# Kernel optimization log

Hardware: AMD Instinct MI355X
Metric: run time of the kernel (lower is better)

The kernel has to match this reference:

```python
import jax, jax.numpy as jnp
import numpy as np
from jax import lax

N_ANCHOR = 9
FEAT_STRIDE = 16
N_PRE_NMS = 2000
N_POST_NMS = 300
NMS_THRESH = 0.7
MIN_SIZE = 16.0
SCALE = 1.0


def generate_anchor(feat_stride, h, w):
    # base anchors: scales {8,16,32} x ratios {0.5,1,2}, (y1,x1,y2,x2)
    base = float(feat_stride)
    ratios = jnp.array([0.5, 1.0, 2.0], jnp.float32)
    scales = jnp.array([8.0, 16.0, 32.0], jnp.float32)
    py = px = base / 2.0
    hs = base * scales[None, :] * jnp.sqrt(ratios)[:, None]          # [3,3]
    ws = base * scales[None, :] * jnp.sqrt(1.0 / ratios)[:, None]    # [3,3]
    anchor_base = jnp.stack([py - hs / 2, px - ws / 2, py + hs / 2, px + ws / 2], axis=-1).reshape(9, 4)
    shift_y = jnp.arange(h, dtype=jnp.float32) * feat_stride
    shift_x = jnp.arange(w, dtype=jnp.float32) * feat_stride
    sy, sx = jnp.meshgrid(shift_y, shift_x, indexing='ij')
    shifts = jnp.stack([sy, sx, sy, sx], axis=-1).reshape(-1, 1, 4)  # [h*w,1,4]
    return (shifts + anchor_base[None]).reshape(-1, 4)               # [h*w*9,4]


def loc2bbox(anchor, loc):
    ah = anchor[:, 2] - anchor[:, 0]
    aw = anchor[:, 3] - anchor[:, 1]
    acy = anchor[:, 0] + 0.5 * ah
    acx = anchor[:, 1] + 0.5 * aw
    dy, dx, dh, dw = loc[:, 0], loc[:, 1], loc[:, 2], loc[:, 3]
    cy = dy * ah + acy
    cx = dx * aw + acx
    h = jnp.exp(dh) * ah
    w = jnp.exp(dw) * aw
    return jnp.stack([cy - 0.5 * h, cx - 0.5 * w, cy + 0.5 * h, cx + 0.5 * w], axis=1)


def nms_keep(boxes, thresh):
    # boxes sorted by descending score; returns keep mask
    y1, x1, y2, x2 = boxes[:, 0], boxes[:, 1], boxes[:, 2], boxes[:, 3]
    area = (y2 - y1) * (x2 - x1)
    yy1 = jnp.maximum(y1[:, None], y1[None, :])
    xx1 = jnp.maximum(x1[:, None], x1[None, :])
    yy2 = jnp.minimum(y2[:, None], y2[None, :])
    xx2 = jnp.minimum(x2[:, None], x2[None, :])
    inter = jnp.clip(yy2 - yy1, 0.0) * jnp.clip(xx2 - xx1, 0.0)
    iou = inter / (area[:, None] + area[None, :] - inter + 1e-9)
    n = boxes.shape[0]

    def step(supp, i):
        keep_i = jnp.logical_not(supp[i])
        supp = supp | (keep_i & (iou[i] > thresh))
        return supp, keep_i

    _, keep = lax.scan(step, jnp.zeros((n,), bool), jnp.arange(n))
    return keep


def proposal_single(loc, score, anchor, img_h, img_w):
    roi = loc2bbox(anchor, loc)
    roi = jnp.stack([
        jnp.clip(roi[:, 0], 0.0, img_h),
        jnp.clip(roi[:, 1], 0.0, img_w),
        jnp.clip(roi[:, 2], 0.0, img_h),
        jnp.clip(roi[:, 3], 0.0, img_w)], axis=1)
    hs = roi[:, 2] - roi[:, 0]
    ws = roi[:, 3] - roi[:, 1]
    ms = MIN_SIZE * SCALE
    score = jnp.where((hs >= ms) & (ws >= ms), score, -jnp.inf)
    top_s, idx = lax.top_k(score, N_PRE_NMS)
    boxes = roi[idx]
    keep = nms_keep(boxes, NMS_THRESH) & jnp.isfinite(top_s)
    order = jnp.argsort(jnp.logical_not(keep), stable=True)[:N_POST_NMS]
    out = boxes[order]
    kout = keep[order]
    return jnp.where(kout[:, None], out, 0.0), kout


def _conv(x, w, b, pad):
    y = lax.conv_general_dilated(x, w, (1, 1), pad, dimension_numbers=('NCHW', 'OIHW', 'NCHW'))
    return y + b[None, :, None, None]


def setup_inputs() -> dict:
    key = jax.random.key(0)
    ks = jax.random.split(key, 7)
    n, c, h, w = 8, 512, 64, 64
    x = jax.random.normal(ks[0], (n, c, h, w), jnp.float32)
    conv_w = 0.01 * jax.random.normal(ks[1], (512, c, 3, 3), jnp.float32)
    conv_b = 0.01 * jax.random.normal(ks[2], (512,), jnp.float32)
    score_w = 0.01 * jax.random.normal(ks[3], (2 * N_ANCHOR, 512, 1, 1), jnp.float32)
    score_b = 0.01 * jax.random.normal(ks[4], (2 * N_ANCHOR,), jnp.float32)
    params_w = 0.01 * jax.random.normal(ks[5], (4 * N_ANCHOR, 512, 1, 1), jnp.float32)
    params_b = 0.01 * jax.random.normal(ks[6], (4 * N_ANCHOR,), jnp.float32)
    return {"x": x, "conv_w": conv_w, "conv_b": conv_b, "score_w": score_w, "score_b": score_b,
            "params_w": params_w, "params_b": params_b, "img_h": 1024, "img_w": 1024}


def reference(x, conv_w, conv_b, score_w, score_b, params_w, params_b, img_h, img_w):
    n, _, h, w = x.shape
    anchor = generate_anchor(FEAT_STRIDE, h, w)                       # [h*w*9,4]
    mid = jax.nn.relu(_conv(x, conv_w, conv_b, 'SAME'))               # [n,512,h,w]
    rpn_params = _conv(mid, params_w, params_b, 'VALID')              # [n,36,h,w]
    rpn_params = rpn_params.transpose(0, 2, 3, 1).reshape(n, -1, 4)   # [n,h*w*9,4]
    rpn_score = _conv(mid, score_w, score_b, 'VALID')                 # [n,18,h,w]
    rpn_score = rpn_score.transpose(0, 2, 3, 1).reshape(n, -1, 2)     # [n,h*w*9,2]
    fg_score = jax.nn.softmax(rpn_score, axis=2)[:, :, 1]             # [n,h*w*9]
    rois, keep = jax.vmap(lambda l, s: proposal_single(l, s, anchor, float(img_h), float(img_w)))(rpn_params, fg_score)
    roi_index = jnp.repeat(jnp.arange(n, dtype=jnp.int32), N_POST_NMS)
    rois = rois.reshape(-1, 4)
    return rpn_params, rpn_score, rois, roi_index, anchor


if __name__ == '__main__':
    out = reference(**setup_inputs())
    print([o.shape for o in out])
```

## Files before the change

### kernel.cpp

```cpp
#include <hip/hip_runtime.h>
#include <math.h>

typedef _Float16 f16x8 __attribute__((ext_vector_type(8)));
typedef float f32x4 __attribute__((ext_vector_type(4)));
typedef unsigned long long u64;

#define OUT_PARAMS 0L
#define OUT_SCORE  1179648L
#define OUT_ROIS   1769472L
#define OUT_IDX    1779072L
#define OUT_ANCH   1781472L

#define WS_WT2   0L
#define WS_W2H   27648L
#define WS_W2L   1207296L
#define WS_XT    2386944L
#define WS_MID   19164160L
#define WS_FG    35941376L
#define WS_KEYS  36236288L
#define WS_BOX   36531200L
#define WS_SELK  37710848L
#define WS_SBOX  37727232L
#define WS_SUPP  37792768L

__global__ void k_transpose_w(const float* __restrict__ conv_w,
                              const float* __restrict__ score_w,
                              const float* __restrict__ params_w,
                              _Float16* __restrict__ W2h, _Float16* __restrict__ W2l,
                              float* __restrict__ wt2) {
  int e = blockIdx.x * 256 + threadIdx.x;
  if (e < 9 * 512 * 512) {
    int tap = e >> 18, rem = e & 262143;
    int oc = rem >> 9, c = rem & 511;
    float v = conv_w[(oc * 512 + c) * 9 + tap] * 1024.0f;
    _Float16 h = (_Float16)v;
    W2h[e] = h;
    W2l[e] = (_Float16)(v - (float)h);
  }
  if (e < 512 * 54) {
    int o = e % 54, c = e / 54;
    wt2[e] = (o < 18) ? score_w[o * 512 + c] : params_w[(o - 18) * 512 + c];
  }
}

__global__ __launch_bounds__(256) void k_split_x(const float* __restrict__ x,
                                                 float* __restrict__ Xt) {
  __shared__ float t[64][66];
  const int pxb = blockIdx.x;
  const int c0  = blockIdx.y * 64;
  const int n   = blockIdx.z;
  const int tid = threadIdx.x;
  const int a = tid >> 6, b = tid & 63;
#pragma unroll
  for (int i = 0; i < 16; ++i) {
    int c_l = i * 4 + a;
    t[c_l][b] = x[((size_t)(n * 512 + c0 + c_l) * 4096) + pxb * 64 + b];
  }
  __syncthreads();
#pragma unroll
  for (int i = 0; i < 16; ++i) {
    int px_l = i * 4 + a;
    Xt[((size_t)(n * 4096 + pxb * 64 + px_l) * 512) + c0 + b] = t[b][px_l];
  }
}

__global__ __launch_bounds__(256, 2) void k_conv_mfma(
    const float* __restrict__ Xt, const _Float16* __restrict__ W2h,
    const _Float16* __restrict__ W2l, const float* __restrict__ bias,
    float* __restrict__ mid) {
  __shared__ _Float16 XH[8448];
  __shared__ _Float16 XL[8448];

  const int n   = blockIdx.x >> 5;
  const int rp  = blockIdx.x & 31;
  const int oc0 = blockIdx.y * 128;
  const int tid = threadIdx.x;
  const int lane = tid & 63, wid = tid >> 6;
  const int wm = wid >> 1, wn = wid & 1;
  const int l15 = lane & 15, kg = lane >> 4;

  f32x4 acch[4][4], accl[4][4];
#pragma unroll
  for (int i = 0; i < 4; ++i)
#pragma unroll
    for (int j = 0; j < 4; ++j) {
      acch[i][j] = (f32x4){0.f, 0.f, 0.f, 0.f};
      accl[i][j] = (f32x4){0.f, 0.f, 0.f, 0.f};
    }

  for (int cb = 0; cb < 16; ++cb) {
    __syncthreads();
    for (int u = tid; u < 1056; u += 256) {
      const int px = u >> 2, sd = u & 3;
      const int cg = sd ^ ((px >> 1) & 3);
      const int hrow = px / 66, hcol = px - hrow * 66;
      const int y = rp * 2 - 1 + hrow, xx = hcol - 1;
      float4 v0 = {0.f, 0.f, 0.f, 0.f}, v1 = {0.f, 0.f, 0.f, 0.f};
      if ((unsigned)y < 64u && (unsigned)xx < 64u) {
        const float* s = Xt + (((size_t)(n * 64 + y) * 64 + xx) * 512 + cb * 32 + cg * 8);
        v0 = *(const float4*)s;
        v1 = *(const float4*)(s + 4);
      }
      f16x8 hv, lv;
      float f[8] = {v0.x, v0.y, v0.z, v0.w, v1.x, v1.y, v1.z, v1.w};
#pragma unroll
      for (int e = 0; e < 8; ++e) {
        const float fs = f[e] * 512.0f;
        _Float16 h = (_Float16)fs;
        hv[e] = h;
        lv[e] = (_Float16)(fs - (float)h);
      }
      *(f16x8*)(XH + u * 8) = hv;
      *(f16x8*)(XL + u * 8) = lv;
    }
    __syncthreads();

#pragma unroll
    for (int ky = 0; ky < 3; ++ky) {
#pragma unroll
      for (int kx = 0; kx < 3; ++kx) {
        const int tap = ky * 3 + kx;
        f16x8 ah[4], al[4], bh[4], bl[4];
#pragma unroll
        for (int mf = 0; mf < 4; ++mf) {
          const size_t aoff =
              ((size_t)(tap * 512 + oc0 + wm * 64 + mf * 16 + l15)) * 512 + cb * 32 + kg * 8;
          ah[mf] = *(const f16x8*)(W2h + aoff);
          al[mf] = *(const f16x8*)(W2l + aoff);
        }
#pragma unroll
        for (int nf = 0; nf < 4; ++nf) {
          const int lpx = (wn + ky) * 66 + nf * 16 + l15 + kx;
          const int off = lpx * 32 + ((kg ^ ((lpx >> 1) & 3)) * 8);
          bh[nf] = *(const f16x8*)(XH + off);
          bl[nf] = *(const f16x8*)(XL + off);
        }
#pragma unroll
        for (int mf = 0; mf < 4; ++mf)
#pragma unroll
          for (int nf = 0; nf < 4; ++nf) {
            acch[mf][nf] = __builtin_amdgcn_mfma_f32_16x16x32_f16(ah[mf], bh[nf], acch[mf][nf], 0, 0, 0);
            accl[mf][nf] = __builtin_amdgcn_mfma_f32_16x16x32_f16(ah[mf], bl[nf], accl[mf][nf], 0, 0, 0);
            accl[mf][nf] = __builtin_amdgcn_mfma_f32_16x16x32_f16(al[mf], bh[nf], accl[mf][nf], 0, 0, 0);
          }
      }
    }
  }

  const float inv = 1.0f / (1024.0f * 512.0f);
  const int y = rp * 2 + wn;
#pragma unroll
  for (int mf = 0; mf < 4; ++mf) {
#pragma unroll
    for (int r = 0; r < 4; ++r) {
      const int oc = oc0 + wm * 64 + mf * 16 + kg * 4 + r;
      const float bv = bias[oc];
      float* mp = mid + (((size_t)(n * 512 + oc) * 64 + y) * 64);
#pragma unroll
      for (int nf = 0; nf < 4; ++nf) {
        const int xcol = nf * 16 + l15;
        mp[xcol] = fmaxf((acch[mf][nf][r] + accl[mf][nf][r]) * inv + bv, 0.f);
      }
    }
  }
}

__global__ __launch_bounds__(256) void k_1x1(
    const float* __restrict__ mid, const float* __restrict__ wt2,
    const float* __restrict__ score_b, const float* __restrict__ params_b,
    float* __restrict__ out, float* __restrict__ fg) {
  const int p = blockIdx.x * 256 + threadIdx.x;
  const int n = p >> 12, hw = p & 4095;
  float acc[54];
#pragma unroll
  for (int o = 0; o < 54; ++o) acc[o] = 0.f;
  const float* m = mid + (size_t)n * 512 * 4096 + hw;
  for (int c = 0; c < 512; ++c) {
    const float mv = m[(size_t)c * 4096];
    const float* w = wt2 + c * 54;
#pragma unroll
    for (int o = 0; o < 54; ++o) acc[o] = fmaf(w[o], mv, acc[o]);
  }
#pragma unroll
  for (int o = 0; o < 18; ++o) acc[o] += score_b[o];
#pragma unroll
  for (int o = 0; o < 36; ++o) acc[18 + o] += params_b[o];

  float* so = out + OUT_SCORE + (size_t)n * 73728 + (size_t)hw * 18;
#pragma unroll
  for (int o = 0; o < 18; ++o) so[o] = acc[o];
  float* po = out + OUT_PARAMS + (size_t)n * 147456 + (size_t)hw * 36;
#pragma unroll
  for (int o = 0; o < 36; ++o) po[o] = acc[18 + o];
  float* f = fg + (size_t)n * 36864 + hw * 9;
#pragma unroll
  for (int a = 0; a < 9; ++a) {
    float d = acc[a * 2 + 1] - acc[a * 2 + 0];
    f[a] = 1.f / (1.f + expf(-d));
  }
}

__global__ void k_proposals(const float* __restrict__ out_params,
                            const float* __restrict__ fg,
                            const int* __restrict__ ih_p, const int* __restrict__ iw_p,
                            float* __restrict__ boxes, unsigned int* __restrict__ keys,
                            float* __restrict__ anchor_out) {
  const int g = blockIdx.x * 256 + threadIdx.x;
  if (g >= 8 * 36864) return;
  const int n = g / 36864, i = g % 36864;
  const int hw = i / 9, a = i % 9;
  const float ih = (float)ih_p[0], iw = (float)iw_p[0];
  const float ratios[3] = {0.5f, 1.f, 2.f};
  const float scales[3] = {8.f, 16.f, 32.f};
  const float rr = ratios[a / 3], sc = scales[a % 3];
  const float hs = (16.f * sc) * sqrtf(rr);
  const float ws_ = (16.f * sc) * sqrtf(1.f / rr);
  const float sy = (float)((hw >> 6) * 16);
  const float sx = (float)((hw & 63) * 16);
  const float ay1 = sy + (8.f - hs * 0.5f), ax1 = sx + (8.f - ws_ * 0.5f);
  const float ay2 = sy + (8.f + hs * 0.5f), ax2 = sx + (8.f + ws_ * 0.5f);
  if (n == 0) {
    float4 av; av.x = ay1; av.y = ax1; av.z = ay2; av.w = ax2;
    *(float4*)&anchor_out[(size_t)i * 4] = av;
  }
  const float ah = ay2 - ay1, aw = ax2 - ax1;
  const float acy = ay1 + 0.5f * ah, acx = ax1 + 0.5f * aw;
  const float* loc = out_params + (size_t)n * 147456 + (size_t)i * 4;
  const float dy = loc[0], dx = loc[1], dh = loc[2], dw = loc[3];
  const float cy = dy * ah + acy, cx = dx * aw + acx;
  const float h = expf(dh) * ah, w = expf(dw) * aw;
  const float y1 = fminf(fmaxf(cy - 0.5f * h, 0.f), ih);
  const float x1 = fminf(fmaxf(cx - 0.5f * w, 0.f), iw);
  const float y2 = fminf(fmaxf(cy + 0.5f * h, 0.f), ih);
  const float x2 = fminf(fmaxf(cx + 0.5f * w, 0.f), iw);
  float4 bx; bx.x = y1; bx.y = x1; bx.z = y2; bx.w = x2;
  *(float4*)&boxes[(size_t)g * 4] = bx;
  float s = fg[g];
  if (!((y2 - y1) >= 16.f && (x2 - x1) >= 16.f)) s = -INFINITY;
  const unsigned int b = __float_as_uint(s);
  keys[g] = (b & 0x80000000u) ? ~b : (b | 0x80000000u);
}

__global__ __launch_bounds__(256) void k_select(
    const unsigned int* __restrict__ keys, const float* __restrict__ boxes,
    unsigned int* __restrict__ selkey, float* __restrict__ sboxes) {
  __shared__ unsigned int hist[4][256];
  __shared__ unsigned long long sel[4096];
  __shared__ unsigned int s_prefix, s_remk, s_cnt;
  const int n = blockIdx.x, tid = threadIdx.x;
  const unsigned int* kk = keys + (size_t)n * 36864;
  if (tid == 0) { s_prefix = 0; s_remk = 2000; s_cnt = 0; }
  const int hslot = tid >> 6;

  for (int byte = 3; byte >= 0; --byte) {
    for (int b2 = tid; b2 < 1024; b2 += 256) ((unsigned int*)hist)[b2] = 0;
    __syncthreads();
    const unsigned pfx = s_prefix;
    const unsigned hmask = (byte == 3) ? 0u : (0xFFFFFFFFu << ((byte + 1) * 8));
    for (int i2 = tid; i2 < 36864; i2 += 256) {
      const unsigned k = kk[i2];
      if ((k & hmask) == (pfx & hmask))
        atomicAdd(&hist[hslot][(k >> (byte * 8)) & 255], 1u);
    }
    __syncthreads();
    if (tid == 0) {
      unsigned rem = s_remk;
      int b2 = 255;
      for (;; --b2) {
        const unsigned c2 = hist[0][b2] + hist[1][b2] + hist[2][b2] + hist[3][b2];
        if (c2 >= rem) break;
        rem -= c2;
      }
      s_prefix = pfx | ((unsigned)b2 << (byte * 8));
      s_remk = rem;
    }
    __syncthreads();
  }
  const unsigned T = s_prefix;

  for (int i2 = tid; i2 < 36864; i2 += 256) {
    const unsigned k = kk[i2];
    if (k >= T) {
      const unsigned p2 = atomicAdd(&s_cnt, 1u);
      if (p2 < 4096)
        sel[p2] = ((unsigned long long)k << 32) | (unsigned)(~i2);
    }
  }
  __syncthreads();
  unsigned cnt = s_cnt; if (cnt > 4096) cnt = 4096;
  for (int i2 = (int)cnt + tid; i2 < 4096; i2 += 256) sel[i2] = 0ull;

  for (int k2 = 2; k2 <= 4096; k2 <<= 1) {
    for (int j = k2 >> 1; j > 0; j >>= 1) {
      __syncthreads();
      for (int t = tid; t < 2048; t += 256) {
        const int i1 = (t << 1) - (t & (j - 1));
        const int i2 = i1 + j;
        const unsigned long long va = sel[i1], vb = sel[i2];
        const bool sw = ((i1 & k2) == 0) ? (va < vb) : (va > vb);
        if (sw) { sel[i1] = vb; sel[i2] = va; }
      }
    }
  }
  __syncthreads();

  for (int s2 = tid; s2 < 2048; s2 += 256) {
    const unsigned long long comp = sel[s2];
    unsigned key = (unsigned)(comp >> 32);
    unsigned idx = ~(unsigned)(comp & 0xFFFFFFFFu);
    float4 bx; bx.x = 0.f; bx.y = 0.f; bx.z = 0.f; bx.w = 0.f;
    if (comp != 0ull) bx = *(const float4*)&boxes[((size_t)n * 36864 + idx) * 4];
    else key = 0;
    selkey[n * 2048 + s2] = key;
    *(float4*)&sboxes[((size_t)n * 2048 + s2) * 4] = bx;
  }
}

__global__ void k_nms_matrix(const float* __restrict__ sboxes,
                             unsigned long long* __restrict__ supp) {
  const int t = blockIdx.x * 256 + threadIdx.x;
  if (t >= 8 * 2000 * 32) return;
  const int n = t / 64000, rem = t % 64000;
  const int i = rem >> 5, w = rem & 31;
  const float4 bi = *(const float4*)&sboxes[((size_t)n * 2048 + i) * 4];
  const float areai = (bi.z - bi.x) * (bi.w - bi.y);
  unsigned long long bits = 0ull;
  const int j0 = w * 64;
  for (int jj = 0; jj < 64; ++jj) {
    const int j = j0 + jj;
    if (j >= 2000) break;
    const float4 bj = *(const float4*)&sboxes[((size_t)n * 2048 + j) * 4];
    const float areaj = (bj.z - bj.x) * (bj.w - bj.y);
    const float yy1 = fmaxf(bi.x, bj.x), xx1 = fmaxf(bi.y, bj.y);
    const float yy2 = fminf(bi.z, bj.z), xx2 = fminf(bi.w, bj.w);
    const float ih2 = fmaxf(yy2 - yy1, 0.f), iw2 = fmaxf(xx2 - xx1, 0.f);
    const float inter = ih2 * iw2;
    const float iou = inter / (areai + areaj - inter + 1e-9f);
    if (iou > 0.7f) bits |= (1ull << jj);
  }
  supp[((size_t)n * 2000 + i) * 32 + w] = bits;
}

__global__ void k_nms_scan(const unsigned long long* __restrict__ supp,
                           const unsigned int* __restrict__ selkey,
                           const float* __restrict__ sboxes,
                           float* __restrict__ out) {
  const int n = blockIdx.x;
  const int lane = threadIdx.x;
  const unsigned long long* sp = supp + (size_t)n * 64000;
  const bool ld = lane < 32;
  unsigned long long removed = 0ull, keepmask = 0ull;
#define LDROW(i) (ld ? sp[(size_t)(i) * 32 + lane] : 0ull)
  unsigned long long r0 = LDROW(0), r1 = LDROW(1), r2 = LDROW(2), r3 = LDROW(3),
                     r4 = LDROW(4), r5 = LDROW(5), r6 = LDROW(6), r7 = LDROW(7);
  for (int g = 0; g < 250; ++g) {
    unsigned long long n0 = 0, n1 = 0, n2 = 0, n3 = 0, n4 = 0, n5 = 0, n6 = 0, n7 = 0;
    if (g < 249) {
      const int nb = (g + 1) * 8;
      n0 = LDROW(nb); n1 = LDROW(nb + 1); n2 = LDROW(nb + 2); n3 = LDROW(nb + 3);
      n4 = LDROW(nb + 4); n5 = LDROW(nb + 5); n6 = LDROW(nb + 6); n7 = LDROW(nb + 7);
    }
#define STEP(K, RK)                                                       \
    {                                                                     \
      const int i = g * 8 + K;                                            \
      const unsigned long long remw = __shfl(removed, i >> 6);            \
      if (!((remw >> (i & 63)) & 1ull)) {                                 \
        if (ld) removed |= RK;                                            \
        if (lane == (i >> 6)) keepmask |= (1ull << (i & 63));             \
      }                                                                   \
    }
    STEP(0, r0) STEP(1, r1) STEP(2, r2) STEP(3, r3)
    STEP(4, r4) STEP(5, r5) STEP(6, r6) STEP(7, r7)
#undef STEP
    r0 = n0; r1 = n1; r2 = n2; r3 = n3; r4 = n4; r5 = n5; r6 = n6; r7 = n7;
  }
#undef LDROW
  int running = 0;
  for (int ci = 0; ci < 32; ++ci) {
    const unsigned long long km = __shfl(keepmask, ci);
    const int i = ci * 64 + lane;
    const unsigned key = selkey[n * 2048 + i];
    const bool fin = (key >= 0x80000000u);
    const bool kf = (((km >> lane) & 1ull) != 0ull) && fin;
    const unsigned long long ball = __ballot(kf);
    const int rank = running + __popcll(ball & ((1ull << lane) - 1ull));
    if (kf && rank < 300) {
      const float4 bx = *(const float4*)&sboxes[((size_t)n * 2048 + i) * 4];
      *(float4*)&out[OUT_ROIS + ((size_t)n * 300 + rank) * 4] = bx;
    }
    running += __popcll(ball);
  }
  const int kept = running < 300 ? running : 300;
  for (int r2 = kept + lane; r2 < 300; r2 += 64) {
    float4 z; z.x = 0.f; z.y = 0.f; z.z = 0.f; z.w = 0.f;
    *(float4*)&out[OUT_ROIS + ((size_t)n * 300 + r2) * 4] = z;
  }
  for (int r2 = lane; r2 < 300; r2 += 64)
    out[OUT_IDX + n * 300 + r2] = (float)n;
}

extern "C" void kernel_launch(void* const* d_in, const int* in_sizes, int n_in,
                              void* d_out, int out_size, void* d_ws, size_t ws_size,
                              hipStream_t stream) {
  const float* x        = (const float*)d_in[0];
  const float* conv_w   = (const float*)d_in[1];
  const float* conv_b   = (const float*)d_in[2];
  const float* score_w  = (const float*)d_in[3];
  const float* score_b  = (const float*)d_in[4];
  const float* params_w = (const float*)d_in[5];
  const float* params_b = (const float*)d_in[6];
  const int*   ih       = (const int*)d_in[7];
  const int*   iw       = (const int*)d_in[8];
  float* out = (float*)d_out;
  float* ws  = (float*)d_ws;

  float* wt2 = ws + WS_WT2;
  _Float16* W2h = (_Float16*)(ws + WS_W2H);
  _Float16* W2l = (_Float16*)(ws + WS_W2L);
  float* Xt  = ws + WS_XT;
  float* mid = ws + WS_MID;
  float* fg  = ws + WS_FG;
  unsigned int* keys = (unsigned int*)(ws + WS_KEYS);
  float* boxes = ws + WS_BOX;
  unsigned int* selkey = (unsigned int*)(ws + WS_SELK);
  float* sboxes = ws + WS_SBOX;
  u64* supp = (u64*)(ws + WS_SUPP);

  hipLaunchKernelGGL(k_transpose_w, dim3(9216), dim3(256), 0, stream,
                     conv_w, score_w, params_w, W2h, W2l, wt2);
  hipLaunchKernelGGL(k_split_x, dim3(64, 8, 8), dim3(256), 0, stream, x, Xt);
  hipLaunchKernelGGL(k_conv_mfma, dim3(256, 4), dim3(256), 0, stream,
                     Xt, W2h, W2l, conv_b, mid);
  hipLaunchKernelGGL(k_1x1, dim3(128), dim3(256), 0, stream,
                     mid, wt2, score_b, params_b, out, fg);
  hipLaunchKernelGGL(k_proposals, dim3(1152), dim3(256), 0, stream,
                     out + OUT_PARAMS, fg, ih, iw, boxes, keys, out + OUT_ANCH);
  hipLaunchKernelGGL(k_select, dim3(8), dim3(256), 0, stream,
                     keys, boxes, selkey, sboxes);
  hipLaunchKernelGGL(k_nms_matrix, dim3(2000), dim3(256), 0, stream,
                     sboxes, supp);
  hipLaunchKernelGGL(k_nms_scan, dim3(8), dim3(64), 0, stream,
                     supp, selkey, sboxes, out);
}
```

Baseline: 1.487 ms.

## Pre-split input to padded fp16 hi/lo planes and double-buffer conv staging via direct LDS loads

The input split into fp16 high and low parts moves from the conv inner loop into the transpose kernel, which now writes into a zero-padded 66x66 layout so the conv no longer needs bounds checks. The conv kernel stages tiles with global_load_lds into a double-buffered shared array, overlapping the next channel block's load with the MFMA work, and remaps block indices so work is grouped by XCD. The select kernel also aggregates histogram and counter atomics across each wavefront using ballots. Costs are an extra zero-pad kernel, a shared workspace layout, and twice the LDS per block, which may reduce occupancy.

```diff
diff --git a/kernel.cpp b/kernel.cpp
--- a/kernel.cpp
+++ b/kernel.cpp
@@ -14,14 +14,15 @@
 #define WS_WT2   0L
 #define WS_W2H   27648L
 #define WS_W2L   1207296L
-#define WS_XT    2386944L
-#define WS_MID   19164160L
-#define WS_FG    35941376L
-#define WS_KEYS  36236288L
-#define WS_BOX   36531200L
-#define WS_SELK  37710848L
-#define WS_SBOX  37727232L
-#define WS_SUPP  37792768L
+#define WS_XTH   2386944L
+#define WS_XTL   11308032L
+#define WS_MID   20229120L
+#define WS_FG    2386944L
+#define WS_KEYS  2681856L
+#define WS_BOX   2976768L
+#define WS_SELK  4156416L
+#define WS_SBOX  4172800L
+#define WS_SUPP  4238336L
 
 __global__ void k_transpose_w(const float* __restrict__ conv_w,
                               const float* __restrict__ score_w,
@@ -43,8 +44,27 @@
   }
 }
 
+__global__ void k_zero_pad(_Float16* __restrict__ XtH, _Float16* __restrict__ XtL) {
+  const int t = blockIdx.x * 256 + threadIdx.x;
+  if (t >= 2 * 8 * 260 * 64) return;
+  const int cg = t & 63;
+  const int px_i = (t >> 6) % 260;
+  const int n = ((t >> 6) / 260) & 7;
+  const int plane = t / (64 * 260 * 8);
+  int prow, pcol;
+  if (px_i < 66) { prow = 0; pcol = px_i; }
+  else if (px_i < 132) { prow = 65; pcol = px_i - 66; }
+  else if (px_i < 196) { prow = px_i - 132 + 1; pcol = 0; }
+  else { prow = px_i - 196 + 1; pcol = 65; }
+  _Float16* dst = (plane ? XtL : XtH) +
+                  (((size_t)(n * 66 + prow) * 66) + pcol) * 512 + cg * 8;
+  float4 z = {0.f, 0.f, 0.f, 0.f};
+  *(float4*)dst = z;
+}
+
 __global__ __launch_bounds__(256) void k_split_x(const float* __restrict__ x,
-                                                 float* __restrict__ Xt) {
+                                                 _Float16* __restrict__ XtH,
+                                                 _Float16* __restrict__ XtL) {
   __shared__ float t[64][66];
   const int pxb = blockIdx.x;
   const int c0  = blockIdx.y * 64;
@@ -60,20 +80,27 @@
 #pragma unroll
   for (int i = 0; i < 16; ++i) {
     int px_l = i * 4 + a;
-    Xt[((size_t)(n * 4096 + pxb * 64 + px_l) * 512) + c0 + b] = t[b][px_l];
+    const float fs = t[b][px_l] * 512.0f;
+    const _Float16 h = (_Float16)fs;
+    const _Float16 l = (_Float16)(fs - (float)h);
+    const size_t o = (((size_t)(n * 66 + pxb + 1) * 66) + px_l + 1) * 512 + c0 + b;
+    XtH[o] = h;
+    XtL[o] = l;
   }
 }
 
 __global__ __launch_bounds__(256, 2) void k_conv_mfma(
-    const float* __restrict__ Xt, const _Float16* __restrict__ W2h,
-    const _Float16* __restrict__ W2l, const float* __restrict__ bias,
-    float* __restrict__ mid) {
-  __shared__ _Float16 XH[8448];
-  __shared__ _Float16 XL[8448];
-
-  const int n   = blockIdx.x >> 5;
-  const int rp  = blockIdx.x & 31;
-  const int oc0 = blockIdx.y * 128;
+    const _Float16* __restrict__ XtH, const _Float16* __restrict__ XtL,
+    const _Float16* __restrict__ W2h, const _Float16* __restrict__ W2l,
+    const float* __restrict__ bias, float* __restrict__ mid) {
+  __shared__ _Float16 SX[2][16896];
+
+  const int swz = blockIdx.x;
+  const int xcd = swz & 7, slot = swz >> 3;
+  const int sub = slot * 2 + (xcd & 1);
+  const int n = sub >> 5, rp = sub & 31;
+  const int oc0 = (xcd >> 1) * 128;
+
   const int tid = threadIdx.x;
   const int lane = tid & 63, wid = tid >> 6;
   const int wm = wid >> 1, wn = wid & 1;
@@ -88,32 +115,37 @@
       accl[i][j] = (f32x4){0.f, 0.f, 0.f, 0.f};
     }
 
+  auto stage = [&](int buf, int cb) {
+#pragma unroll
+    for (int u0 = 0; u0 < 9; ++u0) {
+      const int u = u0 * 4 + wid;
+      if (u < 33) {
+        const int e = u * 64 + lane;
+        const int pl = (e >= 1056) ? 1 : 0;
+        const int idx = e - pl * 1056;
+        const int px = idx >> 2, sd = idx & 3;
+        const int cg = sd ^ ((px >> 1) & 3);
+        const int hrow = px / 66;
+        const int hcol = px - hrow * 66;
+        const _Float16* base = pl ? XtL : XtH;
+        const _Float16* g = base +
+            (((size_t)(n * 66 + rp * 2 + hrow) * 66) + hcol) * 512 + cb * 32 + cg * 8;
+        __builtin_amdgcn_global_load_lds(
+            (const __attribute__((address_space(1))) unsigned int*)(const void*)g,
+            (__attribute__((address_space(3))) unsigned int*)(void*)
+                ((char*)(&SX[buf][0]) + u * 1024),
+            16, 0, 0);
+      }
+    }
+  };
+
+  stage(0, 0);
+  __syncthreads();
+
+#pragma unroll 2
   for (int cb = 0; cb < 16; ++cb) {
-    __syncthreads();
-    for (int u = tid; u < 1056; u += 256) {
-      const int px = u >> 2, sd = u & 3;
-      const int cg = sd ^ ((px >> 1) & 3);
-      const int hrow = px / 66, hcol = px - hrow * 66;
-      const int y = rp * 2 - 1 + hrow, xx = hcol - 1;
-      float4 v0 = {0.f, 0.f, 0.f, 0.f}, v1 = {0.f, 0.f, 0.f, 0.f};
-      if ((unsigned)y < 64u && (unsigned)xx < 64u) {
-        const float* s = Xt + (((size_t)(n * 64 + y) * 64 + xx) * 512 + cb * 32 + cg * 8);
-        v0 = *(const float4*)s;
-        v1 = *(const float4*)(s + 4);
-      }
-      f16x8 hv, lv;
-      float f[8] = {v0.x, v0.y, v0.z, v0.w, v1.x, v1.y, v1.z, v1.w};
-#pragma unroll
-      for (int e = 0; e < 8; ++e) {
-        const float fs = f[e] * 512.0f;
-        _Float16 h = (_Float16)fs;
-        hv[e] = h;
-        lv[e] = (_Float16)(fs - (float)h);
-      }
-      *(f16x8*)(XH + u * 8) = hv;
-      *(f16x8*)(XL + u * 8) = lv;
-    }
-    __syncthreads();
+    const int buf = cb & 1;
+    if (cb < 15) stage(buf ^ 1, cb + 1);
 
 #pragma unroll
     for (int ky = 0; ky < 3; ++ky) {
@@ -132,8 +164,8 @@
         for (int nf = 0; nf < 4; ++nf) {
           const int lpx = (wn + ky) * 66 + nf * 16 + l15 + kx;
           const int off = lpx * 32 + ((kg ^ ((lpx >> 1) & 3)) * 8);
-          bh[nf] = *(const f16x8*)(XH + off);
-          bl[nf] = *(const f16x8*)(XL + off);
+          bh[nf] = *(const f16x8*)(&SX[buf][off]);
+          bl[nf] = *(const f16x8*)(&SX[buf][8448 + off]);
         }
 #pragma unroll
         for (int mf = 0; mf < 4; ++mf)
@@ -145,6 +177,7 @@
           }
       }
     }
+    __syncthreads();
   }
 
   const float inv = 1.0f / (1024.0f * 512.0f);
@@ -248,6 +281,7 @@
   __shared__ unsigned long long sel[4096];
   __shared__ unsigned int s_prefix, s_remk, s_cnt;
   const int n = blockIdx.x, tid = threadIdx.x;
+  const int lane = tid & 63;
   const unsigned int* kk = keys + (size_t)n * 36864;
   if (tid == 0) { s_prefix = 0; s_remk = 2000; s_cnt = 0; }
   const int hslot = tid >> 6;
@@ -259,8 +293,18 @@
     const unsigned hmask = (byte == 3) ? 0u : (0xFFFFFFFFu << ((byte + 1) * 8));
     for (int i2 = tid; i2 < 36864; i2 += 256) {
       const unsigned k = kk[i2];
-      if ((k & hmask) == (pfx & hmask))
-        atomicAdd(&hist[hslot][(k >> (byte * 8)) & 255], 1u);
+      if ((k & hmask) == (pfx & hmask)) {
+        const unsigned b8 = (k >> (byte * 8)) & 255u;
+        unsigned long long peers = __ballot(1);
+#pragma unroll
+        for (int bit = 0; bit < 8; ++bit) {
+          const unsigned long long bb = __ballot((b8 >> bit) & 1u);
+          peers &= ((b8 >> bit) & 1u) ? bb : ~bb;
+        }
+        peers &= __ballot(1);
+        if (lane == __builtin_ctzll(peers))
+          atomicAdd(&hist[hslot][b8], (unsigned)__popcll(peers));
+      }
     }
     __syncthreads();
     if (tid == 0) {
@@ -281,7 +325,12 @@
   for (int i2 = tid; i2 < 36864; i2 += 256) {
     const unsigned k = kk[i2];
     if (k >= T) {
-      const unsigned p2 = atomicAdd(&s_cnt, 1u);
+      const unsigned long long m = __ballot(1);
+      const int ldr = __builtin_ctzll(m);
+      unsigned basep = 0;
+      if (lane == ldr) basep = atomicAdd(&s_cnt, (unsigned)__popcll(m));
+      basep = __shfl(basep, ldr);
+      const unsigned p2 = basep + (unsigned)__popcll(m & ((1ull << lane) - 1ull));
       if (p2 < 4096)
         sel[p2] = ((unsigned long long)k << 32) | (unsigned)(~i2);
     }
@@ -417,7 +466,8 @@
   float* wt2 = ws + WS_WT2;
   _Float16* W2h = (_Float16*)(ws + WS_W2H);
   _Float16* W2l = (_Float16*)(ws + WS_W2L);
-  float* Xt  = ws + WS_XT;
+  _Float16* XtH = (_Float16*)(ws + WS_XTH);
+  _Float16* XtL = (_Float16*)(ws + WS_XTL);
   float* mid = ws + WS_MID;
   float* fg  = ws + WS_FG;
   unsigned int* keys = (unsigned int*)(ws + WS_KEYS);
@@ -428,9 +478,10 @@
 
   hipLaunchKernelGGL(k_transpose_w, dim3(9216), dim3(256), 0, stream,
                      conv_w, score_w, params_w, W2h, W2l, wt2);
-  hipLaunchKernelGGL(k_split_x, dim3(64, 8, 8), dim3(256), 0, stream, x, Xt);
-  hipLaunchKernelGGL(k_conv_mfma, dim3(256, 4), dim3(256), 0, stream,
-                     Xt, W2h, W2l, conv_b, mid);
+  hipLaunchKernelGGL(k_zero_pad, dim3(1040), dim3(256), 0, stream, XtH, XtL);
+  hipLaunchKernelGGL(k_split_x, dim3(64, 8, 8), dim3(256), 0, stream, x, XtH, XtL);
+  hipLaunchKernelGGL(k_conv_mfma, dim3(1024), dim3(256), 0, stream,
+                     XtH, XtL, W2h, W2l, conv_b, mid);
   hipLaunchKernelGGL(k_1x1, dim3(128), dim3(256), 0, stream,
                      mid, wt2, score_b, params_b, out, fg);
   hipLaunchKernelGGL(k_proposals, dim3(1152), dim3(256), 0, stream,
```

New measurement: 1.640 ms. 10.3% more time.
